# Optimization experiments

Hardware: AMD Instinct MI355X
Metric: run time of the kernel (lower is better)

Reference implementation:

```python
import jax, jax.numpy as jnp
import numpy as np

SHAPES = [(64, 64), (32, 32), (16, 16), (8, 8)]  # (H, W) per level, sum HW = 5440
DIMS, NH, NLVL, NPTS, D_HEIGHT, NCAM, NQ, BS = 256, 8, 4, 8, 4, 6, 10000, 1


def ms_deform_attn(value, shapes, loc, attw):
    # value [B, sumHW, nH, dh]; loc [B, nq, nH, L, P, 2] in [0,1]; attw [B, nq, nH, L, P]
    B, _, nH, dh = value.shape
    nq, P = loc.shape[1], loc.shape[4]
    out = jnp.zeros((B, nH, nq, dh), value.dtype)
    start = 0
    for lvl, (h, w) in enumerate(shapes):
        v = value[:, start:start + h * w].transpose(0, 2, 1, 3)  # [B,nH,hw,dh]
        start += h * w
        l = loc[:, :, :, lvl].transpose(0, 2, 1, 3, 4)  # [B,nH,nq,P,2]
        x = l[..., 0] * w - 0.5
        y = l[..., 1] * h - 0.5
        x0, y0 = jnp.floor(x), jnp.floor(y)
        acc = jnp.zeros((B, nH, nq, P, dh), value.dtype)
        for dy in (0.0, 1.0):
            for dx in (0.0, 1.0):
                cx, cy = x0 + dx, y0 + dy
                wgt = (1.0 - jnp.abs(x - cx)) * (1.0 - jnp.abs(y - cy))
                valid = (cx >= 0) & (cx < w) & (cy >= 0) & (cy < h)
                xi = jnp.clip(cx, 0, w - 1).astype(jnp.int32)
                yi = jnp.clip(cy, 0, h - 1).astype(jnp.int32)
                idx = (yi * w + xi).reshape(B, nH, -1)  # [B,nH,nq*P]
                g = jnp.take_along_axis(v, idx[..., None], axis=2).reshape(B, nH, nq, P, dh)
                acc = acc + jnp.where(valid, wgt, 0.0)[..., None] * g
        aw = attw[:, :, :, lvl].transpose(0, 2, 1, 3)  # [B,nH,nq,P]
        out = out + jnp.einsum('bhqp,bhqpd->bhqd', aw, acc)
    return out.transpose(0, 2, 1, 3).reshape(B, nq, nH * dh)


def setup_inputs() -> dict:
    key = jax.random.key(0)
    ks = jax.random.split(key, 16)
    l = sum(h * w for h, w in SHAPES)
    s = 1.0 / np.sqrt(DIMS)
    inp = {
        'query': jax.random.normal(ks[0], (BS, NQ, DIMS), jnp.float32),
        'key': jax.random.normal(ks[1], (NCAM, l, BS, DIMS), jnp.float32),
        'value': jax.random.normal(ks[2], (NCAM, l, BS, DIMS), jnp.float32),
        'ref_points': jax.random.uniform(ks[3], (NCAM, BS, NQ, D_HEIGHT, 2), jnp.float32),
        'vox_mask': jax.random.randint(ks[4], (NCAM, BS, NQ, D_HEIGHT), 0, 2) > 0,
        'spatial_shapes': np.array(SHAPES, dtype=np.int64),
        'level_start_index': np.array([0, 4096, 5120, 5376], dtype=np.int64),
        'value_W': jax.random.uniform(ks[5], (DIMS, DIMS), jnp.float32, -s, s),
        'value_b': jnp.zeros((DIMS,), jnp.float32),
        'off_W': jax.random.normal(ks[6], (DIMS, NH * NLVL * NPTS * 2), jnp.float32) * 0.01,
        'off_b': jax.random.normal(ks[7], (NH * NLVL * NPTS * 2,), jnp.float32) * 0.1,
        'attw_W': jax.random.normal(ks[8], (DIMS, NH * NLVL * NPTS), jnp.float32) * 0.02,
        'attw_b': jnp.zeros((NH * NLVL * NPTS,), jnp.float32),
        'out_W': jax.random.uniform(ks[9], (DIMS, DIMS), jnp.float32, -s, s),
        'out_b': jnp.zeros((DIMS,), jnp.float32),
    }
    return inp


def reference(query, key, value, ref_points, vox_mask, spatial_shapes, level_start_index,
              value_W, value_b, off_W, off_b, attw_W, attw_b, out_W, out_b):
    shapes = [(int(h), int(w)) for h, w in np.asarray(spatial_shapes)]
    bs, nq, dims = query.shape
    cam = vox_mask.shape[0]
    B = bs * cam
    nH = NH
    dh = dims // nH
    Lv, P, D = len(shapes), NPTS, ref_points.shape[3]

    # value_proj; key unused by deformable attention math
    v = value.transpose(2, 0, 1, 3).reshape(B, -1, dims)
    v = (v @ value_W + value_b).reshape(B, -1, nH, dh)

    # rebatch: every camera sees the full (batch-0 visible) query set; padded
    # entries in the original are discarded, so computing all and masking is exact.
    q = jnp.broadcast_to(query[:, None], (bs, cam, nq, dims)).reshape(B, nq, dims)

    off = (q @ off_W + off_b).reshape(B, nq, nH, Lv, P, 2)
    attw = jax.nn.softmax((q @ attw_W + attw_b).reshape(B, nq, nH, Lv * P), -1)
    attw = attw.reshape(B, nq, nH, Lv, P)

    norm = jnp.array([[w, h] for h, w in shapes], q.dtype)  # [Lv,2] -> (W,H)
    off = off / norm[None, None, None, :, None, :]

    ref_rb = ref_points.transpose(1, 0, 2, 3, 4).reshape(B, nq, D, 2)
    off = off.reshape(B, nq, nH, Lv, P // D, D, 2)
    loc = (ref_rb[:, :, None, None, None] + off).reshape(B, nq, nH, Lv, P, 2)

    out = ms_deform_attn(v, shapes, loc, attw).reshape(bs, cam, nq, dims)

    valid = (vox_mask[:, 0].sum(-1) > 0).astype(q.dtype)  # [cam,nq] (batch-0 indexes, as original)
    slots = jnp.einsum('cq,bcqd->bqd', valid, out)
    count = (vox_mask.sum(-1) > 0).transpose(1, 2, 0).sum(-1).astype(q.dtype)
    count = jnp.maximum(count, 1.0)
    slots = slots / count[..., None]
    slots = slots @ out_W + out_b
    return slots + query  # dropout = identity (eval); inp_residual = query
```

## Files before the change

### kernel.cpp

```cpp
#include <hip/hip_runtime.h>


typedef unsigned short ushort_t;
typedef unsigned int uint_t;
typedef __attribute__((ext_vector_type(8))) short bf16x8;
typedef __attribute__((ext_vector_type(4))) float f32x4;

__device__ __forceinline__ float bf2f(ushort_t u) {
    return __uint_as_float(((uint_t)u) << 16);
}
__device__ __forceinline__ ushort_t f2bf(float f) {
    uint_t i = __float_as_uint(f);
    uint_t r = i + 0x7fffu + ((i >> 16) & 1u);
    return (ushort_t)(r >> 16);
}

__global__ __launch_bounds__(256) void cvt_bf16(
    const float* __restrict__ src, ushort_t* __restrict__ dst, int n8) {
    const int i = blockIdx.x * 256 + threadIdx.x;
    if (i >= n8) return;
    const float4 v0 = *(const float4*)(src + (size_t)i * 8);
    const float4 v1 = *(const float4*)(src + (size_t)i * 8 + 4);
    const bf16x8 pk = {
        (short)f2bf(v0.x), (short)f2bf(v0.y), (short)f2bf(v0.z), (short)f2bf(v0.w),
        (short)f2bf(v1.x), (short)f2bf(v1.y), (short)f2bf(v1.z), (short)f2bf(v1.w)};
    *(bf16x8*)(dst + (size_t)i * 8) = pk;
}

__global__ __launch_bounds__(256) void transpose_w(
    const float* __restrict__ Wv, const float* __restrict__ Wo,
    const float* __restrict__ Wf, const float* __restrict__ Wa,
    ushort_t* __restrict__ Tv, ushort_t* __restrict__ To,
    ushort_t* __restrict__ Tqk) {
    const int z = blockIdx.z;
    const float* W;
    ushort_t* T;
    int N;
    if (z == 0)      { W = Wv; T = Tv;              N = 256; }
    else if (z == 1) { W = Wo; T = To;              N = 256; }
    else if (z == 2) { W = Wf; T = Tqk;             N = 512; }
    else             { W = Wa; T = Tqk + 512 * 256; N = 256; }
    const int n0 = blockIdx.y * 32;
    if (n0 >= N) return;
    const int k0 = blockIdx.x * 32;

    __shared__ float tile[32][33];
    const int tx = threadIdx.x & 31;
    const int ty = threadIdx.x >> 5;

    #pragma unroll
    for (int r = 0; r < 4; ++r) {
        const int k = ty + r * 8;
        tile[k][tx] = W[(size_t)(k0 + k) * N + n0 + tx];
    }
    __syncthreads();
    #pragma unroll
    for (int r = 0; r < 4; ++r) {
        const int n = ty + r * 8;
        T[(size_t)(n0 + n) * 256 + k0 + tx] = f2bf(tile[tx][n]);
    }
}

template <bool OUT_BF16, bool RESID>
__global__ __launch_bounds__(256) void gemm_mfma(
    const ushort_t* __restrict__ A, const ushort_t* __restrict__ Wt,
    const float* __restrict__ bias0, const float* __restrict__ bias1, int split,
    const float* __restrict__ resid, void* __restrict__ Cv, int M, int N) {
    __shared__ ushort_t sA[2][128][32];
    __shared__ ushort_t sB[2][128][32];

    const int m0 = blockIdx.x * 128;
    const int n0 = blockIdx.y * 128;
    const int t    = threadIdx.x;
    const int lane = t & 63;
    const int w    = t >> 6;
    const int wr   = w >> 1, wc = w & 1;

    const int srow = t >> 2;
    const int skof = (t & 3) * 8;

    const bool am0 = (m0 + srow) < M;
    const bool am1 = (m0 + 64 + srow) < M;
    const ushort_t* Ap0 = A + (size_t)(m0 + srow) * 256 + skof;
    const ushort_t* Ap1 = Ap0 + (size_t)64 * 256;
    const ushort_t* Bp0 = Wt + (size_t)(n0 + srow) * 256 + skof;
    const ushort_t* Bp1 = Bp0 + (size_t)64 * 256;

    f32x4 acc[4][4];
    #pragma unroll
    for (int i = 0; i < 4; ++i)
        #pragma unroll
        for (int j = 0; j < 4; ++j)
            acc[i][j] = (f32x4){0.f, 0.f, 0.f, 0.f};

    const bf16x8 zz = {0, 0, 0, 0, 0, 0, 0, 0};

    {
        const bf16x8 a0 = am0 ? *(const bf16x8*)(Ap0) : zz;
        const bf16x8 a1 = am1 ? *(const bf16x8*)(Ap1) : zz;
        const bf16x8 b0 = *(const bf16x8*)(Bp0);
        const bf16x8 b1 = *(const bf16x8*)(Bp1);
        *(bf16x8*)(&sA[0][srow][skof])      = a0;
        *(bf16x8*)(&sA[0][64 + srow][skof]) = a1;
        *(bf16x8*)(&sB[0][srow][skof])      = b0;
        *(bf16x8*)(&sB[0][64 + srow][skof]) = b1;
    }
    __syncthreads();

    const int rl = lane & 15;
    const int kq = (lane >> 4) * 8;

    for (int k = 0; k < 8; ++k) {
        const int buf = k & 1;

        bf16x8 na0 = zz, na1 = zz, nb0 = zz, nb1 = zz;
        if (k < 7) {
            const int ko = (k + 1) * 32;
            if (am0) na0 = *(const bf16x8*)(Ap0 + ko);
            if (am1) na1 = *(const bf16x8*)(Ap1 + ko);
            nb0 = *(const bf16x8*)(Bp0 + ko);
            nb1 = *(const bf16x8*)(Bp1 + ko);
        }

        bf16x8 af[4], bfr[4];
        #pragma unroll
        for (int i = 0; i < 4; ++i)
            af[i] = *(const bf16x8*)(&sA[buf][wr * 64 + i * 16 + rl][kq]);
        #pragma unroll
        for (int j = 0; j < 4; ++j)
            bfr[j] = *(const bf16x8*)(&sB[buf][wc * 64 + j * 16 + rl][kq]);
        #pragma unroll
        for (int i = 0; i < 4; ++i)
            #pragma unroll
            for (int j = 0; j < 4; ++j)
                acc[i][j] = __builtin_amdgcn_mfma_f32_16x16x32_bf16(
                    af[i], bfr[j], acc[i][j], 0, 0, 0);

        if (k < 7) {
            __syncthreads();
            *(bf16x8*)(&sA[buf ^ 1][srow][skof])      = na0;
            *(bf16x8*)(&sA[buf ^ 1][64 + srow][skof]) = na1;
            *(bf16x8*)(&sB[buf ^ 1][srow][skof])      = nb0;
            *(bf16x8*)(&sB[buf ^ 1][64 + srow][skof]) = nb1;
            __syncthreads();
        }
    }

    const int col_l = lane & 15;
    const int rq    = (lane >> 4) * 4;
    #pragma unroll
    for (int j = 0; j < 4; ++j) {
        const int gn = n0 + wc * 64 + j * 16 + col_l;
        const float bj = (gn < split) ? bias0[gn] : bias1[gn - split];
        #pragma unroll
        for (int i = 0; i < 4; ++i) {
            #pragma unroll
            for (int r = 0; r < 4; ++r) {
                const int gm = m0 + wr * 64 + i * 16 + rq + r;
                if (gm >= M) continue;
                float v = acc[i][j][r] + bj;
                if (RESID) v += resid[(size_t)gm * N + gn];
                if (OUT_BF16)
                    ((ushort_t*)Cv)[(size_t)gm * N + gn] = f2bf(v);
                else
                    ((float*)Cv)[(size_t)gm * N + gn] = v;
            }
        }
    }
}

__global__ __launch_bounds__(256) void sample_k(
    const float* __restrict__ qkcat,
    const float* __restrict__ refp,
    const int* __restrict__ vox,
    const ushort_t* __restrict__ vproj,
    ushort_t* __restrict__ slots) {
    const int q   = blockIdx.x;
    const int tid = threadIdx.x;
    const int h     = tid >> 5;
    const int lp    = tid & 31;
    const int slice = (tid >> 2) & 7;
    const int g     = tid & 3;

    __shared__ float s_valid[8];
    __shared__ int   s_ci[4][256];
    __shared__ float s_cw[4][256];
    __shared__ float s_red[256][8];

    if (tid < 6) {
        const int base = (tid * 10000 + q) * 4;
        const int mm = vox[base] | vox[base + 1] | vox[base + 2] | vox[base + 3];
        s_valid[tid] = mm ? 1.0f : 0.0f;
    }

    const float a = qkcat[(size_t)q * 768 + 512 + tid];
    float mx = a;
    #pragma unroll
    for (int o = 16; o >= 1; o >>= 1) mx = fmaxf(mx, __shfl_xor(mx, o));
    const float e = __expf(a - mx);
    float se = e;
    #pragma unroll
    for (int o = 16; o >= 1; o >>= 1) se += __shfl_xor(se, o);
    const float aw = e / se;

    const int lvl = lp >> 3;
    const int p   = lp & 7;
    const int dd  = p & 3;
    const int   Sarr[4]   = {64, 32, 16, 8};
    const int   Lstart[4] = {0, 4096, 5120, 5376};
    const int   S  = Sarr[lvl];
    const float Sf = (float)S;
    const int   lstart = Lstart[lvl];
    const float ox = qkcat[(size_t)q * 768 + h * 64 + lvl * 16 + p * 2 + 0] / Sf;
    const float oy = qkcat[(size_t)q * 768 + h * 64 + lvl * 16 + p * 2 + 1] / Sf;

    __syncthreads();
    const float cnt = s_valid[0] + s_valid[1] + s_valid[2] +
                      s_valid[3] + s_valid[4] + s_valid[5];

    float acc[8] = {};
    const int gofs = g << 3;

    for (int c = 0; c < 6; ++c) {
        if (s_valid[c] == 0.0f) continue;

        {
            const int rbase = ((c * 10000 + q) * 4 + dd) * 2;
            const float rx = refp[rbase + 0];
            const float ry = refp[rbase + 1];
            const float x  = (rx + ox) * Sf - 0.5f;
            const float y  = (ry + oy) * Sf - 0.5f;
            const float x0 = floorf(x), y0 = floorf(y);
            #pragma unroll
            for (int k = 0; k < 4; ++k) {
                const float cx = x0 + (float)(k & 1);
                const float cy = y0 + (float)(k >> 1);
                const float wgt = (1.0f - fabsf(x - cx)) * (1.0f - fabsf(y - cy));
                const bool ok = (cx >= 0.0f) & (cx < Sf) & (cy >= 0.0f) & (cy < Sf);
                const int xi = (int)fminf(fmaxf(cx, 0.0f), Sf - 1.0f);
                const int yi = (int)fminf(fmaxf(cy, 0.0f), Sf - 1.0f);
                s_ci[k][tid] = (c * 5440 + lstart + yi * S + xi) * 256 + h * 32;
                s_cw[k][tid] = ok ? wgt * aw : 0.0f;
            }
        }
        __syncthreads();

        #pragma unroll
        for (int j = 0; j < 4; ++j) {
            const int el = h * 32 + slice * 4 + j;
            #pragma unroll
            for (int k = 0; k < 4; ++k) {
                const int   idx = s_ci[k][el];
                const float wv  = s_cw[k][el];
                const uint4 v = *(const uint4*)(vproj + idx + gofs);
                acc[0] += wv * __uint_as_float(v.x << 16);
                acc[1] += wv * __uint_as_float(v.x & 0xffff0000u);
                acc[2] += wv * __uint_as_float(v.y << 16);
                acc[3] += wv * __uint_as_float(v.y & 0xffff0000u);
                acc[4] += wv * __uint_as_float(v.z << 16);
                acc[5] += wv * __uint_as_float(v.z & 0xffff0000u);
                acc[6] += wv * __uint_as_float(v.w << 16);
                acc[7] += wv * __uint_as_float(v.w & 0xffff0000u);
            }
        }
        __syncthreads();
    }

    #pragma unroll
    for (int e2 = 0; e2 < 8; ++e2) s_red[tid][e2] = acc[e2];
    __syncthreads();

    const int cch = tid & 31;
    float sum = 0.0f;
    #pragma unroll
    for (int s = 0; s < 8; ++s)
        sum += s_red[h * 32 + s * 4 + (cch >> 3)][cch & 7];

    slots[(size_t)q * 256 + tid] = f2bf(sum / fmaxf(cnt, 1.0f));
}

extern "C" void kernel_launch(void* const* d_in, const int* in_sizes, int n_in,
                              void* d_out, int out_size, void* d_ws, size_t ws_size,
                              hipStream_t stream) {
    const float* query   = (const float*)d_in[0];
    const float* value   = (const float*)d_in[2];
    const float* refp    = (const float*)d_in[3];
    const int*   vox     = (const int*)d_in[4];
    const float* value_W = (const float*)d_in[7];
    const float* value_b = (const float*)d_in[8];
    const float* off_W   = (const float*)d_in[9];
    const float* off_b   = (const float*)d_in[10];
    const float* attw_W  = (const float*)d_in[11];
    const float* attw_b  = (const float*)d_in[12];
    const float* out_W   = (const float*)d_in[13];
    const float* out_b   = (const float*)d_in[14];
    float* out = (float*)d_out;

    char* ws = (char*)d_ws;
    ushort_t* vproj    = (ushort_t*)ws;
    ushort_t* value_bf = (ushort_t*)(ws + 16711680);
    float*    qkcat    = (float*)   (ws + 16711680);
    ushort_t* query_bf = (ushort_t*)(ws + 47431680);
    ushort_t* slots    = (ushort_t*)(ws + 47431680);
    ushort_t* value_Wt = (ushort_t*)(ws + 52551680);
    ushort_t* out_Wt   = (ushort_t*)(ws + 52551680 + 131072);
    ushort_t* qk_Wt    = (ushort_t*)(ws + 52551680 + 262144);

    cvt_bf16<<<4080, 256, 0, stream>>>(value, value_bf, 1044480);
    cvt_bf16<<<1250, 256, 0, stream>>>(query, query_bf, 320000);
    transpose_w<<<dim3(8, 16, 4), 256, 0, stream>>>(
        value_W, out_W, off_W, attw_W, value_Wt, out_Wt, qk_Wt);
    gemm_mfma<true, false><<<dim3(255, 2), 256, 0, stream>>>(
        value_bf, value_Wt, value_b, value_b, 256, nullptr,
        (void*)vproj, 32640, 256);
    gemm_mfma<false, false><<<dim3(79, 6), 256, 0, stream>>>(
        query_bf, qk_Wt, off_b, attw_b, 512, nullptr,
        (void*)qkcat, 10000, 768);
    sample_k<<<10000, 256, 0, stream>>>(qkcat, refp, vox, vproj, slots);
    gemm_mfma<false, true><<<dim3(79, 2), 256, 0, stream>>>(
        slots, out_Wt, out_b, out_b, 256, query, (void*)out, 10000, 256);
}
```

Before: 358.3 us.

## Fuse bf16 conversion into GEMM loads, merge projections, shuffle sample indices

Removes the two standalone fp32-to-bf16 conversion kernels by having the GEMM convert A tiles on load. The value and query projection GEMMs are merged into one launch. In the sampling kernel, per-corner indices and weights now pass between lanes via wave shuffles instead of shared memory plus two barriers per camera, and accumulation uses packed float2 math. This cuts launches, intermediate global traffic and sync overhead. In exchange the GEMM reads twice as many bytes for A and does conversion in its inner loop.

```diff
diff --git a/kernel.cpp b/kernel.cpp
--- a/kernel.cpp
+++ b/kernel.cpp
@@ -5,6 +5,7 @@
 typedef unsigned int uint_t;
 typedef __attribute__((ext_vector_type(8))) short bf16x8;
 typedef __attribute__((ext_vector_type(4))) float f32x4;
+typedef __attribute__((ext_vector_type(2))) float f32x2;
 
 __device__ __forceinline__ float bf2f(ushort_t u) {
     return __uint_as_float(((uint_t)u) << 16);
@@ -14,20 +15,13 @@
     uint_t r = i + 0x7fffu + ((i >> 16) & 1u);
     return (ushort_t)(r >> 16);
 }
-
-__global__ __launch_bounds__(256) void cvt_bf16(
-    const float* __restrict__ src, ushort_t* __restrict__ dst, int n8) {
-    const int i = blockIdx.x * 256 + threadIdx.x;
-    if (i >= n8) return;
-    const float4 v0 = *(const float4*)(src + (size_t)i * 8);
-    const float4 v1 = *(const float4*)(src + (size_t)i * 8 + 4);
-    const bf16x8 pk = {
+__device__ __forceinline__ bf16x8 pack8(float4 v0, float4 v1) {
+    return (bf16x8){
         (short)f2bf(v0.x), (short)f2bf(v0.y), (short)f2bf(v0.z), (short)f2bf(v0.w),
         (short)f2bf(v1.x), (short)f2bf(v1.y), (short)f2bf(v1.z), (short)f2bf(v1.w)};
-    *(bf16x8*)(dst + (size_t)i * 8) = pk;
-}
-
-__global__ __launch_bounds__(256) void transpose_w(
+}
+
+__global__ __launch_bounds__(256) void prep_w(
     const float* __restrict__ Wv, const float* __restrict__ Wo,
     const float* __restrict__ Wf, const float* __restrict__ Wa,
     ushort_t* __restrict__ Tv, ushort_t* __restrict__ To,
@@ -47,7 +41,6 @@
     __shared__ float tile[32][33];
     const int tx = threadIdx.x & 31;
     const int ty = threadIdx.x >> 5;
-
     #pragma unroll
     for (int r = 0; r < 4; ++r) {
         const int k = ty + r * 8;
@@ -61,16 +54,15 @@
     }
 }
 
-template <bool OUT_BF16, bool RESID>
-__global__ __launch_bounds__(256) void gemm_mfma(
-    const ushort_t* __restrict__ A, const ushort_t* __restrict__ Wt,
+template <bool AF32, bool OUT_BF16, bool RESID>
+__device__ __forceinline__ void gemm_body(
+    ushort_t (*sA)[128][32], ushort_t (*sB)[128][32],
+    const void* __restrict__ Av, const ushort_t* __restrict__ Wt,
     const float* __restrict__ bias0, const float* __restrict__ bias1, int split,
-    const float* __restrict__ resid, void* __restrict__ Cv, int M, int N) {
-    __shared__ ushort_t sA[2][128][32];
-    __shared__ ushort_t sB[2][128][32];
-
-    const int m0 = blockIdx.x * 128;
-    const int n0 = blockIdx.y * 128;
+    const float* __restrict__ resid, void* __restrict__ Cv,
+    int M, int N, int bx, int by) {
+    const int m0 = bx * 128;
+    const int n0 = by * 128;
     const int t    = threadIdx.x;
     const int lane = t & 63;
     const int w    = t >> 6;
@@ -81,11 +73,25 @@
 
     const bool am0 = (m0 + srow) < M;
     const bool am1 = (m0 + 64 + srow) < M;
-    const ushort_t* Ap0 = A + (size_t)(m0 + srow) * 256 + skof;
-    const ushort_t* Ap1 = Ap0 + (size_t)64 * 256;
+    const float*    Af0 = (const float*)Av + (size_t)(m0 + srow) * 256 + skof;
+    const float*    Af1 = Af0 + (size_t)64 * 256;
+    const ushort_t* Ab0 = (const ushort_t*)Av + (size_t)(m0 + srow) * 256 + skof;
+    const ushort_t* Ab1 = Ab0 + (size_t)64 * 256;
     const ushort_t* Bp0 = Wt + (size_t)(n0 + srow) * 256 + skof;
     const ushort_t* Bp1 = Bp0 + (size_t)64 * 256;
 
+    const bf16x8 zz = {0, 0, 0, 0, 0, 0, 0, 0};
+
+    auto loadA = [&](const float* af, const ushort_t* ab, int ko, bool ok) -> bf16x8 {
+        if (!ok) return zz;
+        if (AF32) {
+            const float4 v0 = *(const float4*)(af + ko);
+            const float4 v1 = *(const float4*)(af + ko + 4);
+            return pack8(v0, v1);
+        }
+        return *(const bf16x8*)(ab + ko);
+    };
+
     f32x4 acc[4][4];
     #pragma unroll
     for (int i = 0; i < 4; ++i)
@@ -93,11 +99,9 @@
         for (int j = 0; j < 4; ++j)
             acc[i][j] = (f32x4){0.f, 0.f, 0.f, 0.f};
 
-    const bf16x8 zz = {0, 0, 0, 0, 0, 0, 0, 0};
-
     {
-        const bf16x8 a0 = am0 ? *(const bf16x8*)(Ap0) : zz;
-        const bf16x8 a1 = am1 ? *(const bf16x8*)(Ap1) : zz;
+        const bf16x8 a0 = loadA(Af0, Ab0, 0, am0);
+        const bf16x8 a1 = loadA(Af1, Ab1, 0, am1);
         const bf16x8 b0 = *(const bf16x8*)(Bp0);
         const bf16x8 b1 = *(const bf16x8*)(Bp1);
         *(bf16x8*)(&sA[0][srow][skof])      = a0;
@@ -116,8 +120,8 @@
         bf16x8 na0 = zz, na1 = zz, nb0 = zz, nb1 = zz;
         if (k < 7) {
             const int ko = (k + 1) * 32;
-            if (am0) na0 = *(const bf16x8*)(Ap0 + ko);
-            if (am1) na1 = *(const bf16x8*)(Ap1 + ko);
+            na0 = loadA(Af0, Ab0, ko, am0);
+            na1 = loadA(Af1, Ab1, ko, am1);
             nb0 = *(const bf16x8*)(Bp0 + ko);
             nb1 = *(const bf16x8*)(Bp1 + ko);
         }
@@ -169,6 +173,38 @@
     }
 }
 
+__global__ __launch_bounds__(256) void gemm_vqk(
+    const float* __restrict__ value, const ushort_t* __restrict__ value_Wt,
+    const float* __restrict__ value_b, ushort_t* __restrict__ vproj,
+    const float* __restrict__ query, const ushort_t* __restrict__ qk_Wt,
+    const float* __restrict__ off_b, const float* __restrict__ attw_b,
+    float* __restrict__ qkcat) {
+    __shared__ ushort_t sA[2][128][32];
+    __shared__ ushort_t sB[2][128][32];
+    int b = blockIdx.x;
+    if (b < 510) {
+        gemm_body<true, true, false>(sA, sB, value, value_Wt, value_b, value_b,
+                                     256, nullptr, (void*)vproj, 32640, 256,
+                                     b % 255, b / 255);
+    } else {
+        b -= 510;
+        gemm_body<true, false, false>(sA, sB, query, qk_Wt, off_b, attw_b,
+                                      512, nullptr, (void*)qkcat, 10000, 768,
+                                      b % 79, b / 79);
+    }
+}
+
+__global__ __launch_bounds__(256) void gemm_out_k(
+    const ushort_t* __restrict__ slots, const ushort_t* __restrict__ out_Wt,
+    const float* __restrict__ out_b, const float* __restrict__ query,
+    float* __restrict__ out) {
+    __shared__ ushort_t sA[2][128][32];
+    __shared__ ushort_t sB[2][128][32];
+    gemm_body<false, false, true>(sA, sB, slots, out_Wt, out_b, out_b, 256,
+                                  query, (void*)out, 10000, 256,
+                                  blockIdx.x, blockIdx.y);
+}
+
 __global__ __launch_bounds__(256) void sample_k(
     const float* __restrict__ qkcat,
     const float* __restrict__ refp,
@@ -177,14 +213,13 @@
     ushort_t* __restrict__ slots) {
     const int q   = blockIdx.x;
     const int tid = threadIdx.x;
+    const int lane  = tid & 63;
     const int h     = tid >> 5;
     const int lp    = tid & 31;
     const int slice = (tid >> 2) & 7;
     const int g     = tid & 3;
 
     __shared__ float s_valid[8];
-    __shared__ int   s_ci[4][256];
-    __shared__ float s_cw[4][256];
     __shared__ float s_red[256][8];
 
     if (tid < 6) {
@@ -218,12 +253,15 @@
     const float cnt = s_valid[0] + s_valid[1] + s_valid[2] +
                       s_valid[3] + s_valid[4] + s_valid[5];
 
-    float acc[8] = {};
-    const int gofs = g << 3;
+    f32x2 acc2[4] = {{0.f, 0.f}, {0.f, 0.f}, {0.f, 0.f}, {0.f, 0.f}};
+    const ushort_t* vp = vproj + (g << 3);
+    const int srcbase = (lane & 32) + slice * 4;
 
     for (int c = 0; c < 6; ++c) {
         if (s_valid[c] == 0.0f) continue;
 
+        int   ci0, ci1, ci2, ci3;
+        float cw0, cw1, cw2, cw3;
         {
             const int rbase = ((c * 10000 + q) * 4 + dd) * 2;
             const float rx = refp[rbase + 0];
@@ -231,6 +269,8 @@
             const float x  = (rx + ox) * Sf - 0.5f;
             const float y  = (ry + oy) * Sf - 0.5f;
             const float x0 = floorf(x), y0 = floorf(y);
+            int   ci[4];
+            float cw[4];
             #pragma unroll
             for (int k = 0; k < 4; ++k) {
                 const float cx = x0 + (float)(k & 1);
@@ -239,35 +279,49 @@
                 const bool ok = (cx >= 0.0f) & (cx < Sf) & (cy >= 0.0f) & (cy < Sf);
                 const int xi = (int)fminf(fmaxf(cx, 0.0f), Sf - 1.0f);
                 const int yi = (int)fminf(fmaxf(cy, 0.0f), Sf - 1.0f);
-                s_ci[k][tid] = (c * 5440 + lstart + yi * S + xi) * 256 + h * 32;
-                s_cw[k][tid] = ok ? wgt * aw : 0.0f;
+                ci[k] = (c * 5440 + lstart + yi * S + xi) * 256 + h * 32;
+                cw[k] = ok ? wgt * aw : 0.0f;
             }
-        }
-        __syncthreads();
+            ci0 = ci[0]; ci1 = ci[1]; ci2 = ci[2]; ci3 = ci[3];
+            cw0 = cw[0]; cw1 = cw[1]; cw2 = cw[2]; cw3 = cw[3];
+        }
 
         #pragma unroll
         for (int j = 0; j < 4; ++j) {
-            const int el = h * 32 + slice * 4 + j;
-            #pragma unroll
-            for (int k = 0; k < 4; ++k) {
-                const int   idx = s_ci[k][el];
-                const float wv  = s_cw[k][el];
-                const uint4 v = *(const uint4*)(vproj + idx + gofs);
-                acc[0] += wv * __uint_as_float(v.x << 16);
-                acc[1] += wv * __uint_as_float(v.x & 0xffff0000u);
-                acc[2] += wv * __uint_as_float(v.y << 16);
-                acc[3] += wv * __uint_as_float(v.y & 0xffff0000u);
-                acc[4] += wv * __uint_as_float(v.z << 16);
-                acc[5] += wv * __uint_as_float(v.z & 0xffff0000u);
-                acc[6] += wv * __uint_as_float(v.w << 16);
-                acc[7] += wv * __uint_as_float(v.w & 0xffff0000u);
-            }
-        }
-        __syncthreads();
-    }
-
-    #pragma unroll
-    for (int e2 = 0; e2 < 8; ++e2) s_red[tid][e2] = acc[e2];
+            const int src = srcbase + j;
+            const int i0 = __shfl(ci0, src), i1 = __shfl(ci1, src);
+            const int i2 = __shfl(ci2, src), i3 = __shfl(ci3, src);
+            const uint4 v0 = *(const uint4*)(vp + i0);
+            const uint4 v1 = *(const uint4*)(vp + i1);
+            const uint4 v2 = *(const uint4*)(vp + i2);
+            const uint4 v3 = *(const uint4*)(vp + i3);
+            const float w0 = __shfl(cw0, src), w1 = __shfl(cw1, src);
+            const float w2 = __shfl(cw2, src), w3 = __shfl(cw3, src);
+            const f32x2 W0 = {w0, w0}, W1 = {w1, w1}, W2 = {w2, w2}, W3 = {w3, w3};
+            acc2[0] += W0 * (f32x2){__uint_as_float(v0.x << 16), __uint_as_float(v0.x & 0xffff0000u)};
+            acc2[1] += W0 * (f32x2){__uint_as_float(v0.y << 16), __uint_as_float(v0.y & 0xffff0000u)};
+            acc2[2] += W0 * (f32x2){__uint_as_float(v0.z << 16), __uint_as_float(v0.z & 0xffff0000u)};
+            acc2[3] += W0 * (f32x2){__uint_as_float(v0.w << 16), __uint_as_float(v0.w & 0xffff0000u)};
+            acc2[0] += W1 * (f32x2){__uint_as_float(v1.x << 16), __uint_as_float(v1.x & 0xffff0000u)};
+            acc2[1] += W1 * (f32x2){__uint_as_float(v1.y << 16), __uint_as_float(v1.y & 0xffff0000u)};
+            acc2[2] += W1 * (f32x2){__uint_as_float(v1.z << 16), __uint_as_float(v1.z & 0xffff0000u)};
+            acc2[3] += W1 * (f32x2){__uint_as_float(v1.w << 16), __uint_as_float(v1.w & 0xffff0000u)};
+            acc2[0] += W2 * (f32x2){__uint_as_float(v2.x << 16), __uint_as_float(v2.x & 0xffff0000u)};
+            acc2[1] += W2 * (f32x2){__uint_as_float(v2.y << 16), __uint_as_float(v2.y & 0xffff0000u)};
+            acc2[2] += W2 * (f32x2){__uint_as_float(v2.z << 16), __uint_as_float(v2.z & 0xffff0000u)};
+            acc2[3] += W2 * (f32x2){__uint_as_float(v2.w << 16), __uint_as_float(v2.w & 0xffff0000u)};
+            acc2[0] += W3 * (f32x2){__uint_as_float(v3.x << 16), __uint_as_float(v3.x & 0xffff0000u)};
+            acc2[1] += W3 * (f32x2){__uint_as_float(v3.y << 16), __uint_as_float(v3.y & 0xffff0000u)};
+            acc2[2] += W3 * (f32x2){__uint_as_float(v3.z << 16), __uint_as_float(v3.z & 0xffff0000u)};
+            acc2[3] += W3 * (f32x2){__uint_as_float(v3.w << 16), __uint_as_float(v3.w & 0xffff0000u)};
+        }
+    }
+
+    #pragma unroll
+    for (int n = 0; n < 4; ++n) {
+        s_red[tid][2 * n]     = acc2[n].x;
+        s_red[tid][2 * n + 1] = acc2[n].y;
+    }
     __syncthreads();
 
     const int cch = tid & 31;
@@ -298,25 +352,16 @@
 
     char* ws = (char*)d_ws;
     ushort_t* vproj    = (ushort_t*)ws;
-    ushort_t* value_bf = (ushort_t*)(ws + 16711680);
     float*    qkcat    = (float*)   (ws + 16711680);
-    ushort_t* query_bf = (ushort_t*)(ws + 47431680);
     ushort_t* slots    = (ushort_t*)(ws + 47431680);
     ushort_t* value_Wt = (ushort_t*)(ws + 52551680);
     ushort_t* out_Wt   = (ushort_t*)(ws + 52551680 + 131072);
     ushort_t* qk_Wt    = (ushort_t*)(ws + 52551680 + 262144);
 
-    cvt_bf16<<<4080, 256, 0, stream>>>(value, value_bf, 1044480);
-    cvt_bf16<<<1250, 256, 0, stream>>>(query, query_bf, 320000);
-    transpose_w<<<dim3(8, 16, 4), 256, 0, stream>>>(
+    prep_w<<<dim3(8, 16, 4), 256, 0, stream>>>(
         value_W, out_W, off_W, attw_W, value_Wt, out_Wt, qk_Wt);
-    gemm_mfma<true, false><<<dim3(255, 2), 256, 0, stream>>>(
-        value_bf, value_Wt, value_b, value_b, 256, nullptr,
-        (void*)vproj, 32640, 256);
-    gemm_mfma<false, false><<<dim3(79, 6), 256, 0, stream>>>(
-        query_bf, qk_Wt, off_b, attw_b, 512, nullptr,
-        (void*)qkcat, 10000, 768);
+    gemm_vqk<<<984, 256, 0, stream>>>(value, value_Wt, value_b, vproj,
+                                      query, qk_Wt, off_b, attw_b, qkcat);
     sample_k<<<10000, 256, 0, stream>>>(qkcat, refp, vox, vproj, slots);
-    gemm_mfma<false, true><<<dim3(79, 2), 256, 0, stream>>>(
-        slots, out_Wt, out_b, out_b, 256, query, (void*)out, 10000, 256);
-}
+    gemm_out_k<<<dim3(79, 2), 256, 0, stream>>>(slots, out_Wt, out_b, query, out);
+}
```

After: 335.3 us. 1.07x faster.
